# Optimization experiments

Measured on AMD Instinct MI355X. Metric: run time of the kernel, lower is better.

## Reference

```python
import jax, jax.numpy as jnp
import numpy as np

N_NODES = 100000
N_EDGES = 1600000
D_FEAT = 64


def setup_inputs() -> dict:
    key = jax.random.key(0)
    k1, k2 = jax.random.split(key)
    x = jax.random.normal(k1, (N_NODES, D_FEAT), dtype=jnp.float32)
    edge_index = jax.random.randint(k2, (2, N_EDGES), 0, N_NODES, dtype=jnp.int64)
    return {"x": x, "edge_index": edge_index}


def reference(x, edge_index):
    # GCNProp (improved=False): remove self loops, add self loops w/ weight 1,
    # symmetric deg^-1/2 normalization, then spmm aggregation.
    N = x.shape[0]
    row, col = edge_index[0], edge_index[1]
    # remove_self_loops: zero the weight of any self-loop edge (math-equivalent
    # to dropping it, and jit-friendly: no data-dependent shapes).
    w = jnp.where(row != col, jnp.ones((), x.dtype), jnp.zeros((), x.dtype))
    # add_self_loops: append N diagonal edges with loop_value = 1 (improved=False)
    loop = jnp.arange(N, dtype=row.dtype)
    row_a = jnp.concatenate([row, loop])          # [E+N]
    col_a = jnp.concatenate([col, loop])          # [E+N]
    w_a = jnp.concatenate([w, jnp.ones((N,), x.dtype)])  # [E+N]
    # degree via scatter_add over rows
    deg = jax.ops.segment_sum(w_a, row_a, num_segments=N)  # [N]
    # deg^-0.5 with inf -> 0
    dinv = jnp.where(deg > 0, jax.lax.rsqrt(deg), jnp.zeros((), x.dtype))
    # edge normalization: deg[row]^-1/2 * w * deg[col]^-1/2
    norm = dinv[row_a] * w_a * dinv[col_a]        # [E+N]
    # spmm: gather neighbor features, scale, scatter-add into rows
    out = jax.ops.segment_sum(norm[:, None] * x[col_a], row_a, num_segments=N)  # [N, D]
    return out
```

## Files before the change

kernel.cpp:

```cpp
#include <hip/hip_runtime.h>

#define N_NODES 100000
#define N_EDGES 1600000
#define D 64
#define NB 391
#define BCAP 4480
#define PBLK 256
#define TPB 512
#define CHUNK ((N_EDGES + PBLK - 1) / PBLK)
#define CURSTRIDE 32

__device__ __forceinline__ unsigned short f2b(float f) {
    unsigned u = __float_as_uint(f);
    u += 0x7FFF + ((u >> 16) & 1);
    return (unsigned short)(u >> 16);
}
__device__ __forceinline__ float b2f(unsigned short v) {
    return __uint_as_float(((unsigned)v) << 16);
}

__global__ void init_cursor_kernel(int* __restrict__ cursor) {
    int b = blockIdx.x * blockDim.x + threadIdx.x;
    if (b < NB) cursor[b * CURSTRIDE] = b * BCAP;
}

__global__ void scatter_direct_kernel(const int* __restrict__ ei, int* __restrict__ cursor,
                                      int* __restrict__ epack) {
    __shared__ int h[NB];
    __shared__ int lbase[NB];
    __shared__ int lcur[NB];
    int t = threadIdx.x;
    for (int i = t; i < NB; i += TPB) h[i] = 0;
    __syncthreads();
    int s = blockIdx.x * CHUNK;
    int e = min(s + CHUNK, N_EDGES);
    for (int i = s + t; i < e; i += TPB) {
        int r = ei[i], c = ei[N_EDGES + i];
        if (r != c) atomicAdd(&h[r >> 8], 1);
    }
    __syncthreads();
    for (int i = t; i < NB; i += TPB) {
        lbase[i] = atomicAdd(&cursor[i * CURSTRIDE], h[i]);
        lcur[i] = 0;
    }
    __syncthreads();
    for (int i = s + t; i < e; i += TPB) {
        int r = ei[i], c = ei[N_EDGES + i];
        if (r != c) {
            int b = r >> 8;
            int p = lbase[b] + atomicAdd(&lcur[b], 1);
            epack[p] = ((r & 255) << 17) | c;
        }
    }
}

__global__ void rowsort_convert_kernel(const int* __restrict__ cursor, int* __restrict__ epack,
                                       int* __restrict__ rowstart, int* __restrict__ rowend,
                                       float* __restrict__ dinv, const float* __restrict__ x,
                                       unsigned short* __restrict__ xs) {
    __shared__ int ebuf[BCAP];
    __shared__ int h[256];
    __shared__ int sc[256];
    __shared__ int cur[256];
    __shared__ float dv[256];
    int b = blockIdx.x;
    int t = threadIdx.x;
    int base = b * BCAP;
    int n = min(cursor[b * CURSTRIDE] - base, BCAP);
    for (int i = t; i < n; i += 256) ebuf[i] = epack[base + i];
    h[t] = 0;
    __syncthreads();
    for (int i = t; i < n; i += 256) atomicAdd(&h[ebuf[i] >> 17], 1);
    __syncthreads();
    int v = h[t];
    sc[t] = v;
    __syncthreads();
    for (int off = 1; off < 256; off <<= 1) {
        int u = (t >= off) ? sc[t - off] : 0;
        __syncthreads();
        sc[t] += u;
        __syncthreads();
    }
    int excl = sc[t] - v;
    int row = b * 256 + t;
    float di = rsqrtf((float)(1 + v));
    if (row < N_NODES) {
        rowstart[row] = base + excl;
        rowend[row] = base + excl + v;
        dinv[row] = di;
    }
    dv[t] = di;
    cur[t] = excl;
    __syncthreads();
    for (int i = t; i < n; i += 256) {
        int p = ebuf[i];
        int pos = atomicAdd(&cur[p >> 17], 1);
        epack[base + pos] = p & 0x1FFFF;
    }
    int nrows = min(256, N_NODES - b * 256);
    const float4* x4 = (const float4*)x;
    ushort4* xs4 = (ushort4*)xs;
    for (int i = t; i < nrows * 16; i += 256) {
        int rl = i >> 4;
        float4 vv = x4[(size_t)(b * 256 + rl) * 16 + (i & 15)];
        float dd = dv[rl];
        ushort4 o;
        o.x = f2b(vv.x * dd);
        o.y = f2b(vv.y * dd);
        o.z = f2b(vv.z * dd);
        o.w = f2b(vv.w * dd);
        xs4[(size_t)(b * 256 + rl) * 16 + (i & 15)] = o;
    }
}

__global__ void gather_kernel(const unsigned short* __restrict__ xs, const float* __restrict__ dinv,
                              const int* __restrict__ rowstart, const int* __restrict__ rowend,
                              const int* __restrict__ sortedCol, float* __restrict__ out) {
    int t = blockIdx.x * blockDim.x + threadIdx.x;
    int r = t >> 6;
    int d = t & 63;
    if (r >= N_NODES) return;
    int start = rowstart[r];
    int end = rowend[r];
    float dr = dinv[r];
    float acc = b2f(xs[r * D + d]);
    for (int j = start; j < end; j += 64) {
        int idx = j + d;
        int cj = 0;
        if (idx < end) cj = sortedCol[idx];
        int n = min(64, end - j);
        int k = 0;
        for (; k + 8 <= n; k += 8) {
            int c0 = __shfl(cj, k);
            int c1 = __shfl(cj, k + 1);
            int c2 = __shfl(cj, k + 2);
            int c3 = __shfl(cj, k + 3);
            int c4 = __shfl(cj, k + 4);
            int c5 = __shfl(cj, k + 5);
            int c6 = __shfl(cj, k + 6);
            int c7 = __shfl(cj, k + 7);
            float v0 = b2f(xs[c0 * D + d]);
            float v1 = b2f(xs[c1 * D + d]);
            float v2 = b2f(xs[c2 * D + d]);
            float v3 = b2f(xs[c3 * D + d]);
            float v4 = b2f(xs[c4 * D + d]);
            float v5 = b2f(xs[c5 * D + d]);
            float v6 = b2f(xs[c6 * D + d]);
            float v7 = b2f(xs[c7 * D + d]);
            acc += ((v0 + v1) + (v2 + v3)) + ((v4 + v5) + (v6 + v7));
        }
        for (; k + 4 <= n; k += 4) {
            int c0 = __shfl(cj, k);
            int c1 = __shfl(cj, k + 1);
            int c2 = __shfl(cj, k + 2);
            int c3 = __shfl(cj, k + 3);
            float v0 = b2f(xs[c0 * D + d]);
            float v1 = b2f(xs[c1 * D + d]);
            float v2 = b2f(xs[c2 * D + d]);
            float v3 = b2f(xs[c3 * D + d]);
            acc += (v0 + v1) + (v2 + v3);
        }
        for (; k < n; k++) {
            int c = __shfl(cj, k);
            acc += b2f(xs[c * D + d]);
        }
    }
    out[r * D + d] = dr * acc;
}

extern "C" void kernel_launch(void* const* d_in, const int* in_sizes, int n_in,
                              void* d_out, int out_size, void* d_ws, size_t ws_size,
                              hipStream_t stream) {
    const float* x = (const float*)d_in[0];
    const int* ei = (const int*)d_in[1];
    float* out = (float*)d_out;

    int* cursor = (int*)d_ws;
    int* rowstart = cursor + NB * CURSTRIDE;
    int* rowend = rowstart + N_NODES;
    float* dinv = (float*)(rowend + N_NODES);
    int* epack = (int*)(dinv + N_NODES);
    unsigned short* xs = (unsigned short*)(epack + NB * BCAP);

    init_cursor_kernel<<<(NB + 255) / 256, 256, 0, stream>>>(cursor);
    scatter_direct_kernel<<<PBLK, TPB, 0, stream>>>(ei, cursor, epack);
    rowsort_convert_kernel<<<NB, 256, 0, stream>>>(cursor, epack, rowstart, rowend, dinv, x, xs);
    gather_kernel<<<(N_NODES * D + 255) / 256, 256, 0, stream>>>(xs, dinv, rowstart, rowend, epack, out);
}
```

Baseline: 159.2 us.

## Replace bucketed two-level sort with global per-row histogram and atomic placement

Builds the CSR with a global per-row atomic histogram, a per-block scan that takes a global offset from an atomic counter, and a second edge pass that places column indices through per-row atomic cursors. This replaces the earlier scheme of bucket scatter followed by a per-bucket shared-memory sort. Edge index reads are vectorised as int4, and dinv is recomputed inside the gather from the row count. The cost is many more global atomics spread over 100k counters, an extra kernel launch, and neighbour order within a row that changes from run to run, so floating-point summation order is no longer deterministic.

Result: slower. 333.3 us (+109.3%).

```diff
diff --git a/kernel.cpp b/kernel.cpp
--- a/kernel.cpp
+++ b/kernel.cpp
@@ -4,11 +4,7 @@
 #define N_EDGES 1600000
 #define D 64
 #define NB 391
-#define BCAP 4480
-#define PBLK 256
-#define TPB 512
-#define CHUNK ((N_EDGES + PBLK - 1) / PBLK)
-#define CURSTRIDE 32
+#define R1 100096
 
 __device__ __forceinline__ unsigned short f2b(float f) {
     unsigned u = __float_as_uint(f);
@@ -19,60 +15,33 @@
     return __uint_as_float(((unsigned)v) << 16);
 }
 
-__global__ void init_cursor_kernel(int* __restrict__ cursor) {
-    int b = blockIdx.x * blockDim.x + threadIdx.x;
-    if (b < NB) cursor[b * CURSTRIDE] = b * BCAP;
+__global__ void zero_kernel(int* __restrict__ p) {
+    int i = blockIdx.x * blockDim.x + threadIdx.x;
+    if (i < R1) p[i] = 0;
 }
 
-__global__ void scatter_direct_kernel(const int* __restrict__ ei, int* __restrict__ cursor,
-                                      int* __restrict__ epack) {
-    __shared__ int h[NB];
-    __shared__ int lbase[NB];
-    __shared__ int lcur[NB];
-    int t = threadIdx.x;
-    for (int i = t; i < NB; i += TPB) h[i] = 0;
-    __syncthreads();
-    int s = blockIdx.x * CHUNK;
-    int e = min(s + CHUNK, N_EDGES);
-    for (int i = s + t; i < e; i += TPB) {
-        int r = ei[i], c = ei[N_EDGES + i];
-        if (r != c) atomicAdd(&h[r >> 8], 1);
-    }
-    __syncthreads();
-    for (int i = t; i < NB; i += TPB) {
-        lbase[i] = atomicAdd(&cursor[i * CURSTRIDE], h[i]);
-        lcur[i] = 0;
-    }
-    __syncthreads();
-    for (int i = s + t; i < e; i += TPB) {
-        int r = ei[i], c = ei[N_EDGES + i];
-        if (r != c) {
-            int b = r >> 8;
-            int p = lbase[b] + atomicAdd(&lcur[b], 1);
-            epack[p] = ((r & 255) << 17) | c;
-        }
-    }
+__global__ void hist_kernel(const int* __restrict__ ei, int* __restrict__ rowcnt) {
+    int t = blockIdx.x * blockDim.x + threadIdx.x;
+    int i4 = t * 4;
+    if (i4 >= N_EDGES) return;
+    int4 r = *(const int4*)(ei + i4);
+    int4 c = *(const int4*)(ei + N_EDGES + i4);
+    if (r.x != c.x) atomicAdd(&rowcnt[r.x], 1);
+    if (r.y != c.y) atomicAdd(&rowcnt[r.y], 1);
+    if (r.z != c.z) atomicAdd(&rowcnt[r.z], 1);
+    if (r.w != c.w) atomicAdd(&rowcnt[r.w], 1);
 }
 
-__global__ void rowsort_convert_kernel(const int* __restrict__ cursor, int* __restrict__ epack,
-                                       int* __restrict__ rowstart, int* __restrict__ rowend,
-                                       float* __restrict__ dinv, const float* __restrict__ x,
-                                       unsigned short* __restrict__ xs) {
-    __shared__ int ebuf[BCAP];
-    __shared__ int h[256];
+__global__ void finalize_convert_kernel(const int* __restrict__ rowcnt, int* __restrict__ gctr,
+                                        int* __restrict__ rowstart, int* __restrict__ cursor,
+                                        const float* __restrict__ x,
+                                        unsigned short* __restrict__ xs) {
     __shared__ int sc[256];
-    __shared__ int cur[256];
     __shared__ float dv[256];
-    int b = blockIdx.x;
-    int t = threadIdx.x;
-    int base = b * BCAP;
-    int n = min(cursor[b * CURSTRIDE] - base, BCAP);
-    for (int i = t; i < n; i += 256) ebuf[i] = epack[base + i];
-    h[t] = 0;
-    __syncthreads();
-    for (int i = t; i < n; i += 256) atomicAdd(&h[ebuf[i] >> 17], 1);
-    __syncthreads();
-    int v = h[t];
+    __shared__ int sbase;
+    int b = blockIdx.x, t = threadIdx.x;
+    int row = b * 256 + t;
+    int v = (row < N_NODES) ? rowcnt[row] : 0;
     sc[t] = v;
     __syncthreads();
     for (int off = 1; off < 256; off <<= 1) {
@@ -81,22 +50,11 @@
         sc[t] += u;
         __syncthreads();
     }
-    int excl = sc[t] - v;
-    int row = b * 256 + t;
-    float di = rsqrtf((float)(1 + v));
-    if (row < N_NODES) {
-        rowstart[row] = base + excl;
-        rowend[row] = base + excl + v;
-        dinv[row] = di;
-    }
-    dv[t] = di;
-    cur[t] = excl;
+    if (t == 255) sbase = atomicAdd(gctr, sc[255]);
+    dv[t] = rsqrtf((float)(1 + v));
     __syncthreads();
-    for (int i = t; i < n; i += 256) {
-        int p = ebuf[i];
-        int pos = atomicAdd(&cur[p >> 17], 1);
-        epack[base + pos] = p & 0x1FFFF;
-    }
+    int rs = sbase + sc[t] - v;
+    if (row < N_NODES) { rowstart[row] = rs; cursor[row] = rs; }
     int nrows = min(256, N_NODES - b * 256);
     const float4* x4 = (const float4*)x;
     ushort4* xs4 = (ushort4*)xs;
@@ -113,21 +71,41 @@
     }
 }
 
-__global__ void gather_kernel(const unsigned short* __restrict__ xs, const float* __restrict__ dinv,
-                              const int* __restrict__ rowstart, const int* __restrict__ rowend,
-                              const int* __restrict__ sortedCol, float* __restrict__ out) {
+__global__ void place_kernel(const int* __restrict__ ei, int* __restrict__ cursor,
+                             int* __restrict__ colidx) {
+    int t = blockIdx.x * blockDim.x + threadIdx.x;
+    int i4 = t * 4;
+    if (i4 >= N_EDGES) return;
+    int4 r = *(const int4*)(ei + i4);
+    int4 c = *(const int4*)(ei + N_EDGES + i4);
+    int p0 = (r.x != c.x) ? atomicAdd(&cursor[r.x], 1) : -1;
+    int p1 = (r.y != c.y) ? atomicAdd(&cursor[r.y], 1) : -1;
+    int p2 = (r.z != c.z) ? atomicAdd(&cursor[r.z], 1) : -1;
+    int p3 = (r.w != c.w) ? atomicAdd(&cursor[r.w], 1) : -1;
+    if (p0 >= 0) colidx[p0] = c.x;
+    if (p1 >= 0) colidx[p1] = c.y;
+    if (p2 >= 0) colidx[p2] = c.z;
+    if (p3 >= 0) colidx[p3] = c.w;
+}
+
+__global__ void gather_kernel(const unsigned short* __restrict__ xs,
+                              const int* __restrict__ rowcnt,
+                              const int* __restrict__ rowstart,
+                              const int* __restrict__ colidx,
+                              float* __restrict__ out) {
     int t = blockIdx.x * blockDim.x + threadIdx.x;
     int r = t >> 6;
     int d = t & 63;
     if (r >= N_NODES) return;
     int start = rowstart[r];
-    int end = rowend[r];
-    float dr = dinv[r];
+    int cnt = rowcnt[r];
+    int end = start + cnt;
+    float dr = rsqrtf((float)(1 + cnt));
     float acc = b2f(xs[r * D + d]);
     for (int j = start; j < end; j += 64) {
         int idx = j + d;
         int cj = 0;
-        if (idx < end) cj = sortedCol[idx];
+        if (idx < end) cj = colidx[idx];
         int n = min(64, end - j);
         int k = 0;
         for (; k + 8 <= n; k += 8) {
@@ -175,15 +153,18 @@
     const int* ei = (const int*)d_in[1];
     float* out = (float*)d_out;
 
-    int* cursor = (int*)d_ws;
-    int* rowstart = cursor + NB * CURSTRIDE;
-    int* rowend = rowstart + N_NODES;
-    float* dinv = (float*)(rowend + N_NODES);
-    int* epack = (int*)(dinv + N_NODES);
-    unsigned short* xs = (unsigned short*)(epack + NB * BCAP);
+    int* rowcnt = (int*)d_ws;
+    int* gctr = rowcnt + N_NODES;
+    int* rowstart = rowcnt + R1;
+    int* cursor = rowstart + N_NODES;
+    int* colidx = cursor + N_NODES;
+    unsigned short* xs = (unsigned short*)(colidx + N_EDGES);
 
-    init_cursor_kernel<<<(NB + 255) / 256, 256, 0, stream>>>(cursor);
-    scatter_direct_kernel<<<PBLK, TPB, 0, stream>>>(ei, cursor, epack);
-    rowsort_convert_kernel<<<NB, 256, 0, stream>>>(cursor, epack, rowstart, rowend, dinv, x, xs);
-    gather_kernel<<<(N_NODES * D + 255) / 256, 256, 0, stream>>>(xs, dinv, rowstart, rowend, epack, out);
+    int egrid = (N_EDGES / 4 + 255) / 256;
+
+    zero_kernel<<<(R1 + 255) / 256, 256, 0, stream>>>(rowcnt);
+    hist_kernel<<<egrid, 256, 0, stream>>>(ei, rowcnt);
+    finalize_convert_kernel<<<NB, 256, 0, stream>>>(rowcnt, gctr, rowstart, cursor, x, xs);
+    place_kernel<<<egrid, 256, 0, stream>>>(ei, cursor, colidx);
+    gather_kernel<<<(N_NODES * D + 255) / 256, 256, 0, stream>>>(xs, rowcnt, rowstart, colidx, out);
 }
```
